# Kernel tuning notes

Hardware: AMD Instinct MI355X
Metric: run time of the kernel (lower is better)

## Reference

```python
import jax, jax.numpy as jnp
import numpy as np

B, T, C, HS = 4, 2048, 1024, 64

def setup_inputs() -> dict:
    key = jax.random.key(0)
    k1, k2, k3, k4 = jax.random.split(key, 4)
    # weights stored as [n_embd, head_size] so projection is x @ W
    scale = C ** -0.5
    return {
        "x": jax.random.normal(k1, (B, T, C), dtype=jnp.float32),
        "Wq": jax.random.normal(k2, (C, HS), dtype=jnp.float32) * scale,
        "Wk": jax.random.normal(k3, (C, HS), dtype=jnp.float32) * scale,
        "Wv": jax.random.normal(k4, (C, HS), dtype=jnp.float32) * scale,
    }

def reference(x, Wq, Wk, Wv):
    # single-head causal attention: softmax(QK^T / sqrt(hs)) V, dropout p=0 (eval)
    q = x @ Wq  # [B,T,hs]
    k = x @ Wk
    v = x @ Wv
    hs = k.shape[-1]
    wei = jnp.einsum('bqh,bkh->bqk', q, k) * (hs ** -0.5)  # [B,T,T]
    causal = jnp.tril(jnp.ones((q.shape[1], q.shape[1]), dtype=bool))
    wei = jnp.where(causal[None, :, :], wei, -jnp.inf)
    wei = jax.nn.softmax(wei, axis=-1)
    out = jnp.einsum('bqk,bkh->bqh', wei, v)  # [B,T,hs]
    return out
```

## Files before the change

kernel.cpp:

```cpp
#include <hip/hip_runtime.h>
#include <stdint.h>

#define NB 4
#define NT 2048
#define NC 1024
#define NH 64
#define NM (NB*NT)

typedef unsigned short u16;
typedef unsigned int u32;
typedef __bf16 bf16_t;
typedef float f32x4 __attribute__((ext_vector_type(4)));
typedef bf16_t bf16x8 __attribute__((ext_vector_type(8)));
typedef u16 u16x8 __attribute__((ext_vector_type(8)));
typedef u16 u16x4 __attribute__((ext_vector_type(4)));

__device__ __forceinline__ u16 f2b(float f) {
  return __builtin_bit_cast(u16, (bf16_t)f);
}

__device__ __forceinline__ void gl16(const void* g, void* l) {
  __builtin_amdgcn_global_load_lds(
      (const __attribute__((address_space(1))) u32*)g,
      (__attribute__((address_space(3))) u32*)l, 16, 0, 0);
}

__global__ __launch_bounds__(256) void wt_kernel(const float* __restrict__ Wq,
                                                 const float* __restrict__ Wk,
                                                 const float* __restrict__ Wv,
                                                 u16* __restrict__ wt) {
  __shared__ float t[64][65];
  const int m = blockIdx.x >> 4;
  const int kt = blockIdx.x & 15;
  const int k0 = kt * 64;
  const float* W = (m == 0) ? Wq : (m == 1) ? Wk : Wv;
  {
    const int r = threadIdx.x >> 2, c4 = threadIdx.x & 3;
    #pragma unroll
    for (int j = 0; j < 4; ++j) {
      const float4 f = *(const float4*)(W + (size_t)(k0 + r) * NH + c4 * 16 + j * 4);
      t[r][c4 * 16 + j * 4 + 0] = f.x;
      t[r][c4 * 16 + j * 4 + 1] = f.y;
      t[r][c4 * 16 + j * 4 + 2] = f.z;
      t[r][c4 * 16 + j * 4 + 3] = f.w;
    }
  }
  __syncthreads();
  const int n = threadIdx.x >> 2, kc = threadIdx.x & 3;
  u16x8 a, b;
  #pragma unroll
  for (int j = 0; j < 8; ++j) a[j] = f2b(t[kc * 16 + j][n]);
  #pragma unroll
  for (int j = 0; j < 8; ++j) b[j] = f2b(t[kc * 16 + 8 + j][n]);
  u16* dst = wt + ((size_t)(m * 64 + n)) * NC + k0 + kc * 16;
  *(u16x8*)dst = a;
  *(u16x8*)(dst + 8) = b;
}

__global__ __launch_bounds__(256, 2) void proj_kernel(const float* __restrict__ x,
                                                      const u16* __restrict__ wt,
                                                      u16* __restrict__ qo,
                                                      u16* __restrict__ ko,
                                                      u16* __restrict__ vto) {
  __shared__ float fA[2][16 * 64];
  __shared__ u16 sB[2][192 * 64];
  const int tid = threadIdx.x;
  const int lane = tid & 63;
  const int w = tid >> 6;
  const int g = lane >> 4;
  const int li = lane & 15;
  const int row0 = blockIdx.x * 16;
  const int wbase = tid & 0xC0;

  const f32x4 zero = {0.f, 0.f, 0.f, 0.f};
  f32x4 acc[3];
  #pragma unroll
  for (int i = 0; i < 3; ++i) acc[i] = zero;

  const int ar = tid >> 4;
  const int ac = tid & 15;
  const float* asrc0 = x + (size_t)(row0 + ar) * NC + ((ac ^ (ar & 7)) * 4);

  auto stage = [&](int kt, int nxt) {
    const int k0 = kt * 64;
    gl16(asrc0 + k0, (char*)fA[nxt] + wbase * 16);
    #pragma unroll
    for (int j = 0; j < 6; ++j) {
      const int cid = j * 256 + tid;
      const int n = cid >> 3, c = cid & 7;
      gl16(wt + (size_t)n * NC + k0 + ((c ^ (n & 7)) * 8),
           (char*)sB[nxt] + (j * 256 + wbase) * 16);
    }
  };

  stage(0, 0);
  __syncthreads();

  for (int kt = 0; kt < 16; ++kt) {
    const int cur = kt & 1;
    if (kt < 15) stage(kt + 1, cur ^ 1);
    #pragma unroll
    for (int ks = 0; ks < 2; ++ks) {
      const int c0 = ks * 8 + g * 2;
      const f32x4 a0 = *(const f32x4*)&fA[cur][li * 64 + ((c0 ^ (li & 7)) * 4)];
      const f32x4 a1 = *(const f32x4*)&fA[cur][li * 64 + (((c0 + 1) ^ (li & 7)) * 4)];
      bf16x8 a;
      a[0]=(bf16_t)a0.x; a[1]=(bf16_t)a0.y; a[2]=(bf16_t)a0.z; a[3]=(bf16_t)a0.w;
      a[4]=(bf16_t)a1.x; a[5]=(bf16_t)a1.y; a[6]=(bf16_t)a1.z; a[7]=(bf16_t)a1.w;
      #pragma unroll
      for (int f = 0; f < 3; ++f) {
        const int n = (w * 3 + f) * 16 + li;
        const bf16x8 b = *(const bf16x8*)&sB[cur][n * 64 + (((ks * 4 + g) ^ (n & 7)) * 8)];
        acc[f] = __builtin_amdgcn_mfma_f32_16x16x32_bf16(a, b, acc[f], 0, 0, 0);
      }
    }
    __syncthreads();
  }

  const int rr0 = row0 + g * 4;
  #pragma unroll
  for (int f = 0; f < 3; ++f) {
    const int fn = w * 3 + f;
    if (fn < 4) {
      #pragma unroll
      for (int i = 0; i < 4; ++i)
        qo[(size_t)(rr0 + i) * NH + fn * 16 + li] = f2b(acc[f][i]);
    } else if (fn < 8) {
      #pragma unroll
      for (int i = 0; i < 4; ++i)
        ko[(size_t)(rr0 + i) * NH + (fn - 4) * 16 + li] = f2b(acc[f][i]);
    } else {
      u16x4 pv;
      #pragma unroll
      for (int i = 0; i < 4; ++i) pv[i] = f2b(acc[f][i]);
      const int hs = (fn - 8) * 16 + li;
      const int bidx = rr0 >> 11;
      const int tt = rr0 & 2047;
      const int tile = tt >> 6, off = tt & 63;
      *(u16x4*)&vto[(((size_t)(bidx * 32 + tile) * 64) + hs) * 64 + off] = pv;
    }
  }
}

struct AttnGrp {
  union {
    struct { u16 K[2][32 * 64]; u16 V[2][64 * 32]; } st;
    struct { float mo[2][16][64]; float ml[2][16]; } mg;
  } u;
};

__global__ __launch_bounds__(512) void attn_kernel(const u16* __restrict__ qg,
                                                   const u16* __restrict__ kg,
                                                   const u16* __restrict__ vtg,
                                                   float* __restrict__ out) {
  __shared__ AttnGrp grp[8];
  __shared__ u16 sP[8][16 * 32];
  const int tid = threadIdx.x;
  const int lane = tid & 63;
  const int s = tid >> 3 >> 3;
  const int g = lane >> 4;
  const int li = lane & 15;
  const int jA = blockIdx.x & 63;
  const int bb = blockIdx.x >> 6;
  const int jB = 127 - jA;
  const size_t bt0 = (size_t)bb * NT;
  const int q0A = jA * 16, q0B = jB * 16;
  const int n1 = (jA >> 1) + 1;

  bf16x8 aqA[2], aqB[2];
  #pragma unroll
  for (int ks = 0; ks < 2; ++ks) {
    aqA[ks] = *(const bf16x8*)(qg + (bt0 + q0A + li) * NH + ks * 32 + g * 8);
    aqB[ks] = *(const bf16x8*)(qg + (bt0 + q0B + li) * NH + ks * 32 + g * 8);
  }

  const f32x4 zero = {0.f, 0.f, 0.f, 0.f};
  f32x4 oA[4], oB[4];
  float lA[4], lB[4];
  #pragma unroll
  for (int i = 0; i < 4; ++i) { oA[i] = zero; oB[i] = zero; lA[i] = 0.f; lB[i] = 0.f; }

  auto stage = [&](int v, int b) {
    const int kvt = (v < n1) ? v : v - n1;
    const size_t kbase = bt0 + (size_t)kvt * 32;
    #pragma unroll
    for (int jj = 0; jj < 4; ++jj) {
      const int idx = jj * 64 + lane;
      const int n = idx >> 3, c = idx & 7;
      gl16(kg + (kbase + n) * NH + ((c ^ (n & 7)) * 8),
           (char*)grp[s].u.st.K[b] + jj * 1024);
    }
    const size_t vbase = ((size_t)(bb * 32 + (kvt >> 1))) * 64;
    const int hoff = (kvt & 1) * 32;
    #pragma unroll
    for (int jj = 0; jj < 4; ++jj) {
      const int idx = jj * 64 + lane;
      const int n = idx >> 2, c = idx & 3;
      gl16(vtg + (vbase + n) * 64 + hoff + ((c ^ (n & 3) ^ ((n >> 2) & 3)) * 8),
           (char*)grp[s].u.st.V[b] + jj * 1024);
    }
  };

  auto computeT = [&](const bf16x8 (&aq)[2], f32x4 (&o)[4], float (&ls)[4],
                      int q0, int kv0, int b) {
    f32x4 sc2[2] = {zero, zero};
    #pragma unroll
    for (int ks = 0; ks < 2; ++ks) {
      #pragma unroll
      for (int fn = 0; fn < 2; ++fn) {
        const int n = fn * 16 + li;
        const bf16x8 bk = *(const bf16x8*)&grp[s].u.st.K[b][n * 64 + (((ks * 4 + g) ^ (n & 7)) * 8)];
        sc2[fn] = __builtin_amdgcn_mfma_f32_16x16x32_bf16(aq[ks], bk, sc2[fn], 0, 0, 0);
      }
    }
    const bool needmask = (kv0 + 31 > q0);
    #pragma unroll
    for (int fn = 0; fn < 2; ++fn) {
      #pragma unroll
      for (int i = 0; i < 4; ++i) {
        const int q = g * 4 + i;
        float v = sc2[fn][i] * 0.125f;
        if (needmask && (kv0 + fn * 16 + li > q0 + q)) v = -1e30f;
        const float e = __expf(v);
        ls[i] += e;
        const int kc = fn * 2 + (li >> 3);
        sP[s][q * 32 + ((kc ^ (q & 3) ^ ((q >> 2) & 3)) * 8) + (li & 7)] = f2b(e);
      }
    }
    const bf16x8 pa = *(const bf16x8*)&sP[s][li * 32 + ((g ^ (li & 3) ^ ((li >> 2) & 3)) * 8)];
    #pragma unroll
    for (int fn = 0; fn < 4; ++fn) {
      const int n = fn * 16 + li;
      const bf16x8 bv = *(const bf16x8*)&grp[s].u.st.V[b][n * 32 + ((g ^ (n & 3) ^ ((n >> 2) & 3)) * 8)];
      o[fn] = __builtin_amdgcn_mfma_f32_16x16x32_bf16(pa, bv, o[fn], 0, 0, 0);
    }
  };

  const int nt = (64 - s) / 8 + 1;
  int v = s;
  stage(v, 0);
  for (int k = 0; k < nt; ++k) {
    if (k + 1 < nt) {
      stage(v + 8, (k + 1) & 1);
      asm volatile("s_waitcnt vmcnt(8)" ::: "memory");
    } else {
      asm volatile("s_waitcnt vmcnt(0)" ::: "memory");
    }
    const int b = k & 1;
    if (v < n1) computeT(aqA, oA, lA, q0A, v * 32, b);
    else        computeT(aqB, oB, lB, q0B, (v - n1) * 32, b);
    v += 8;
  }

  #pragma unroll
  for (int i = 0; i < 4; ++i) {
    float a = lA[i], c = lB[i];
    a += __shfl_xor(a, 1); c += __shfl_xor(c, 1);
    a += __shfl_xor(a, 2); c += __shfl_xor(c, 2);
    a += __shfl_xor(a, 4); c += __shfl_xor(c, 4);
    a += __shfl_xor(a, 8); c += __shfl_xor(c, 8);
    lA[i] = a; lB[i] = c;
  }

  #pragma unroll
  for (int fn = 0; fn < 4; ++fn) {
    #pragma unroll
    for (int i = 0; i < 4; ++i) {
      grp[s].u.mg.mo[0][g * 4 + i][fn * 16 + li] = oA[fn][i];
      grp[s].u.mg.mo[1][g * 4 + i][fn * 16 + li] = oB[fn][i];
    }
  }
  if (li == 0) {
    #pragma unroll
    for (int i = 0; i < 4; ++i) {
      grp[s].u.mg.ml[0][g * 4 + i] = lA[i];
      grp[s].u.mg.ml[1][g * 4 + i] = lB[i];
    }
  }
  __syncthreads();

  {
    const int base = tid * 4;
    const int tile = base >> 10;
    const int r = (base >> 6) & 15;
    const int c0 = base & 63;
    float L = 0.f;
    f32x4 acc = zero;
    #pragma unroll
    for (int s8 = 0; s8 < 8; ++s8) {
      L += grp[s8].u.mg.ml[tile][r];
      acc += *(const f32x4*)&grp[s8].u.mg.mo[tile][r][c0];
    }
    const int row = (tile ? q0B : q0A) + r;
    const float inv = 1.f / L;
    acc *= inv;
    *(f32x4*)&out[(bt0 + row) * NH + c0] = acc;
  }
}

extern "C" void kernel_launch(void* const* d_in, const int* in_sizes, int n_in,
                              void* d_out, int out_size, void* d_ws, size_t ws_size,
                              hipStream_t stream) {
  (void)in_sizes; (void)n_in; (void)out_size; (void)ws_size;
  const float* x  = (const float*)d_in[0];
  const float* Wq = (const float*)d_in[1];
  const float* Wk = (const float*)d_in[2];
  const float* Wv = (const float*)d_in[3];
  float* out = (float*)d_out;
  char* ws = (char*)d_ws;
  u16* qb  = (u16*)(ws);
  u16* kb  = (u16*)(ws + (1u << 20));
  u16* vtb = (u16*)(ws + (2u << 20));
  u16* wtb = (u16*)(ws + (3u << 20));
  hipLaunchKernelGGL(wt_kernel,   dim3(48),  dim3(256), 0, stream, Wq, Wk, Wv, wtb);
  hipLaunchKernelGGL(proj_kernel, dim3(512), dim3(256), 0, stream, x, wtb, qb, kb, vtb);
  hipLaunchKernelGGL(attn_kernel, dim3(256), dim3(512), 0, stream, qb, kb, vtb, out);
}
```

Measured before the change: 38.45 us.

## Split projection GEMM across Q/K/V with a second grid dimension

The projection kernel now launches a 512x3 grid in which each block computes only one of Q, K or V (64 output columns) instead of all 192. Each block stages a 64-row weight slice, so LDS use per block drops and three times as many blocks run. The cost is that each x tile is read three times from global memory and converted to bf16 three times, which raises read traffic on x.

```diff
diff --git a/kernel.cpp b/kernel.cpp
--- a/kernel.cpp
+++ b/kernel.cpp
@@ -57,25 +57,25 @@
   *(u16x8*)(dst + 8) = b;
 }
 
-__global__ __launch_bounds__(256, 2) void proj_kernel(const float* __restrict__ x,
-                                                      const u16* __restrict__ wt,
-                                                      u16* __restrict__ qo,
-                                                      u16* __restrict__ ko,
-                                                      u16* __restrict__ vto) {
+__global__ __launch_bounds__(256) void proj_kernel(const float* __restrict__ x,
+                                                   const u16* __restrict__ wt,
+                                                   u16* __restrict__ qo,
+                                                   u16* __restrict__ ko,
+                                                   u16* __restrict__ vto) {
   __shared__ float fA[2][16 * 64];
-  __shared__ u16 sB[2][192 * 64];
+  __shared__ u16 sB[2][64 * 64];
   const int tid = threadIdx.x;
   const int lane = tid & 63;
   const int w = tid >> 6;
   const int g = lane >> 4;
   const int li = lane & 15;
   const int row0 = blockIdx.x * 16;
+  const int m = blockIdx.y;
   const int wbase = tid & 0xC0;
+  const u16* wslice = wt + (size_t)m * 64 * NC;
 
   const f32x4 zero = {0.f, 0.f, 0.f, 0.f};
-  f32x4 acc[3];
-  #pragma unroll
-  for (int i = 0; i < 3; ++i) acc[i] = zero;
+  f32x4 acc = zero;
 
   const int ar = tid >> 4;
   const int ac = tid & 15;
@@ -85,11 +85,11 @@
     const int k0 = kt * 64;
     gl16(asrc0 + k0, (char*)fA[nxt] + wbase * 16);
     #pragma unroll
-    for (int j = 0; j < 6; ++j) {
+    for (int j = 0; j < 2; ++j) {
       const int cid = j * 256 + tid;
       const int n = cid >> 3, c = cid & 7;
-      gl16(wt + (size_t)n * NC + k0 + ((c ^ (n & 7)) * 8),
-           (char*)sB[nxt] + (j * 256 + wbase) * 16);
+      gl16(wslice + (size_t)n * NC + k0 + ((c ^ (n & 7)) * 8),
+           (char*)sB[nxt] + (j * 4096 + wbase * 16));
     }
   };
 
@@ -107,38 +107,31 @@
       bf16x8 a;
       a[0]=(bf16_t)a0.x; a[1]=(bf16_t)a0.y; a[2]=(bf16_t)a0.z; a[3]=(bf16_t)a0.w;
       a[4]=(bf16_t)a1.x; a[5]=(bf16_t)a1.y; a[6]=(bf16_t)a1.z; a[7]=(bf16_t)a1.w;
-      #pragma unroll
-      for (int f = 0; f < 3; ++f) {
-        const int n = (w * 3 + f) * 16 + li;
-        const bf16x8 b = *(const bf16x8*)&sB[cur][n * 64 + (((ks * 4 + g) ^ (n & 7)) * 8)];
-        acc[f] = __builtin_amdgcn_mfma_f32_16x16x32_bf16(a, b, acc[f], 0, 0, 0);
-      }
+      const int n = w * 16 + li;
+      const bf16x8 b = *(const bf16x8*)&sB[cur][n * 64 + (((ks * 4 + g) ^ (n & 7)) * 8)];
+      acc = __builtin_amdgcn_mfma_f32_16x16x32_bf16(a, b, acc, 0, 0, 0);
     }
     __syncthreads();
   }
 
   const int rr0 = row0 + g * 4;
-  #pragma unroll
-  for (int f = 0; f < 3; ++f) {
-    const int fn = w * 3 + f;
-    if (fn < 4) {
-      #pragma unroll
-      for (int i = 0; i < 4; ++i)
-        qo[(size_t)(rr0 + i) * NH + fn * 16 + li] = f2b(acc[f][i]);
-    } else if (fn < 8) {
-      #pragma unroll
-      for (int i = 0; i < 4; ++i)
-        ko[(size_t)(rr0 + i) * NH + (fn - 4) * 16 + li] = f2b(acc[f][i]);
-    } else {
-      u16x4 pv;
-      #pragma unroll
-      for (int i = 0; i < 4; ++i) pv[i] = f2b(acc[f][i]);
-      const int hs = (fn - 8) * 16 + li;
-      const int bidx = rr0 >> 11;
-      const int tt = rr0 & 2047;
-      const int tile = tt >> 6, off = tt & 63;
-      *(u16x4*)&vto[(((size_t)(bidx * 32 + tile) * 64) + hs) * 64 + off] = pv;
-    }
+  if (m == 0) {
+    #pragma unroll
+    for (int i = 0; i < 4; ++i)
+      qo[(size_t)(rr0 + i) * NH + w * 16 + li] = f2b(acc[i]);
+  } else if (m == 1) {
+    #pragma unroll
+    for (int i = 0; i < 4; ++i)
+      ko[(size_t)(rr0 + i) * NH + w * 16 + li] = f2b(acc[i]);
+  } else {
+    u16x4 pv;
+    #pragma unroll
+    for (int i = 0; i < 4; ++i) pv[i] = f2b(acc[i]);
+    const int hs = w * 16 + li;
+    const int bidx = rr0 >> 11;
+    const int tt = rr0 & 2047;
+    const int tile = tt >> 6, off = tt & 63;
+    *(u16x4*)&vto[(((size_t)(bidx * 32 + tile) * 64) + hs) * 64 + off] = pv;
   }
 }
 
@@ -312,7 +305,7 @@
   u16* kb  = (u16*)(ws + (1u << 20));
   u16* vtb = (u16*)(ws + (2u << 20));
   u16* wtb = (u16*)(ws + (3u << 20));
-  hipLaunchKernelGGL(wt_kernel,   dim3(48),  dim3(256), 0, stream, Wq, Wk, Wv, wtb);
-  hipLaunchKernelGGL(proj_kernel, dim3(512), dim3(256), 0, stream, x, wtb, qb, kb, vtb);
-  hipLaunchKernelGGL(attn_kernel, dim3(256), dim3(512), 0, stream, qb, kb, vtb, out);
-}
+  hipLaunchKernelGGL(wt_kernel,   dim3(48),      dim3(256), 0, stream, Wq, Wk, Wv, wtb);
+  hipLaunchKernelGGL(proj_kernel, dim3(512, 3),  dim3(256), 0, stream, x, wtb, qb, kb, vtb);
+  hipLaunchKernelGGL(attn_kernel, dim3(256),     dim3(512), 0, stream, qb, kb, vtb, out);
+}
```

Measured after the change: 37.59 us. 2.2% less time.

## Share each KV tile between both query blocks and load V fragments directly

Applied to the files above, without the earlier changes.

The loop now runs over the key/value tiles of the later query block. Each staged K tile is reused for the earlier block whenever that tile is causally visible to it, so each K/V tile is fetched once per workgroup instead of once per query block. V is no longer staged through LDS: each wave loads its MFMA B-operand fragments straight from global memory into registers, and the LDS union shrinks to K only. The trade-offs are V load latency that is only partly hidden behind the QK step, and uneven per-iteration work across waves, since some iterations compute one block and others compute two.

```diff
diff --git a/kernel.cpp b/kernel.cpp
--- a/kernel.cpp
+++ b/kernel.cpp
@@ -144,7 +144,7 @@
 
 struct AttnGrp {
   union {
-    struct { u16 K[2][32 * 64]; u16 V[2][64 * 32]; } st;
+    u16 K[2][32 * 64];
     struct { float mo[2][16][64]; float ml[2][16]; } mg;
   } u;
 };
@@ -157,7 +157,7 @@
   __shared__ u16 sP[8][16 * 32];
   const int tid = threadIdx.x;
   const int lane = tid & 63;
-  const int s = tid >> 3 >> 3;
+  const int s = tid >> 6;
   const int g = lane >> 4;
   const int li = lane & 15;
   const int jA = blockIdx.x & 63;
@@ -166,6 +166,7 @@
   const size_t bt0 = (size_t)bb * NT;
   const int q0A = jA * 16, q0B = jB * 16;
   const int n1 = (jA >> 1) + 1;
+  const int nB = 64 - (jA >> 1);
 
   bf16x8 aqA[2], aqB[2];
   #pragma unroll
@@ -180,36 +181,26 @@
   #pragma unroll
   for (int i = 0; i < 4; ++i) { oA[i] = zero; oB[i] = zero; lA[i] = 0.f; lB[i] = 0.f; }
 
-  auto stage = [&](int v, int b) {
-    const int kvt = (v < n1) ? v : v - n1;
-    const size_t kbase = bt0 + (size_t)kvt * 32;
+  auto stageK = [&](int t, int b) {
+    const size_t kbase = bt0 + (size_t)t * 32;
     #pragma unroll
     for (int jj = 0; jj < 4; ++jj) {
       const int idx = jj * 64 + lane;
       const int n = idx >> 3, c = idx & 7;
       gl16(kg + (kbase + n) * NH + ((c ^ (n & 7)) * 8),
-           (char*)grp[s].u.st.K[b] + jj * 1024);
-    }
-    const size_t vbase = ((size_t)(bb * 32 + (kvt >> 1))) * 64;
-    const int hoff = (kvt & 1) * 32;
-    #pragma unroll
-    for (int jj = 0; jj < 4; ++jj) {
-      const int idx = jj * 64 + lane;
-      const int n = idx >> 2, c = idx & 3;
-      gl16(vtg + (vbase + n) * 64 + hoff + ((c ^ (n & 3) ^ ((n >> 2) & 3)) * 8),
-           (char*)grp[s].u.st.V[b] + jj * 1024);
+           (char*)grp[s].u.K[b] + jj * 1024);
     }
   };
 
   auto computeT = [&](const bf16x8 (&aq)[2], f32x4 (&o)[4], float (&ls)[4],
-                      int q0, int kv0, int b) {
+                      int q0, int kv0, int b, const bf16x8 (&vf)[4]) {
     f32x4 sc2[2] = {zero, zero};
     #pragma unroll
     for (int ks = 0; ks < 2; ++ks) {
       #pragma unroll
       for (int fn = 0; fn < 2; ++fn) {
         const int n = fn * 16 + li;
-        const bf16x8 bk = *(const bf16x8*)&grp[s].u.st.K[b][n * 64 + (((ks * 4 + g) ^ (n & 7)) * 8)];
+        const bf16x8 bk = *(const bf16x8*)&grp[s].u.K[b][n * 64 + (((ks * 4 + g) ^ (n & 7)) * 8)];
         sc2[fn] = __builtin_amdgcn_mfma_f32_16x16x32_bf16(aq[ks], bk, sc2[fn], 0, 0, 0);
       }
     }
@@ -229,27 +220,29 @@
     }
     const bf16x8 pa = *(const bf16x8*)&sP[s][li * 32 + ((g ^ (li & 3) ^ ((li >> 2) & 3)) * 8)];
     #pragma unroll
-    for (int fn = 0; fn < 4; ++fn) {
-      const int n = fn * 16 + li;
-      const bf16x8 bv = *(const bf16x8*)&grp[s].u.st.V[b][n * 32 + ((g ^ (n & 3) ^ ((n >> 2) & 3)) * 8)];
-      o[fn] = __builtin_amdgcn_mfma_f32_16x16x32_bf16(pa, bv, o[fn], 0, 0, 0);
-    }
+    for (int fn = 0; fn < 4; ++fn)
+      o[fn] = __builtin_amdgcn_mfma_f32_16x16x32_bf16(pa, vf[fn], o[fn], 0, 0, 0);
   };
 
-  const int nt = (64 - s) / 8 + 1;
-  int v = s;
-  stage(v, 0);
-  for (int k = 0; k < nt; ++k) {
-    if (k + 1 < nt) {
-      stage(v + 8, (k + 1) & 1);
+  stageK(s, 0);
+  int k = 0;
+  for (int t = s; t < nB; t += 8, ++k) {
+    bf16x8 vf[4];
+    const size_t vrow = ((size_t)(bb * 32 + (t >> 1))) * 64;
+    const int hoff = (t & 1) * 32;
+    #pragma unroll
+    for (int fn = 0; fn < 4; ++fn)
+      vf[fn] = *(const bf16x8*)(vtg + (vrow + fn * 16 + li) * 64 + hoff + g * 8);
+
+    if (t + 8 < nB) {
+      stageK(t + 8, (k + 1) & 1);
       asm volatile("s_waitcnt vmcnt(8)" ::: "memory");
     } else {
-      asm volatile("s_waitcnt vmcnt(0)" ::: "memory");
+      asm volatile("s_waitcnt vmcnt(4)" ::: "memory");
     }
     const int b = k & 1;
-    if (v < n1) computeT(aqA, oA, lA, q0A, v * 32, b);
-    else        computeT(aqB, oB, lB, q0B, (v - n1) * 32, b);
-    v += 8;
+    computeT(aqB, oB, lB, q0B, t * 32, b, vf);
+    if (t < n1) computeT(aqA, oA, lA, q0A, t * 32, b, vf);
   }
 
   #pragma unroll
```

Result: no change. 38.55 us (+0.2%).
